# Kernel optimization log

Hardware: AMD Instinct MI355X
Metric: run time of the kernel (lower is better)

Reference implementation:

```python
import jax, jax.numpy as jnp
import numpy as np

G = 256       # number of graphs in batch
NPG = 400     # nodes per graph (hardcoded in module)
DEG = 32      # avg degree
FIN = 400     # input feature dim
H = 64        # hidden_channels
N = G * NPG
E = G * NPG * DEG


def _glorot(key, fan_in, fan_out):
    lim = float(np.sqrt(6.0 / (fan_in + fan_out)))
    return jax.random.uniform(key, (fan_in, fan_out), jnp.float32, -lim, lim)


def setup_inputs() -> dict:
    key = jax.random.key(0)
    ks = jax.random.split(key, 12)
    x = jax.random.normal(ks[0], (N, FIN), jnp.float32)
    # intra-graph random edges, then offset by graph id so edges never cross graphs
    src = jax.random.randint(ks[1], (G, NPG * DEG), 0, NPG)
    dst = jax.random.randint(ks[2], (G, NPG * DEG), 0, NPG)
    offs = (jnp.arange(G) * NPG)[:, None]
    edge_index = jnp.stack([(src + offs).reshape(-1), (dst + offs).reshape(-1)]).astype(jnp.int32)
    edge_weight = jax.random.uniform(ks[3], (E,), jnp.float32)
    return {
        "x": x,
        "edge_index": edge_index,
        "edge_weight": edge_weight,
        "W1": _glorot(ks[4], FIN, H), "b1": jnp.zeros((H,), jnp.float32),
        "W2": _glorot(ks[5], H, H),   "b2": jnp.zeros((H,), jnp.float32),
        "W3": _glorot(ks[6], H, H),   "b3": jnp.zeros((H,), jnp.float32),
        "Wc": _glorot(ks[7], NPG * H, H), "bc": jnp.zeros((H,), jnp.float32),
        "Wl": _glorot(ks[8], H, 2),   "bl": jnp.zeros((2,), jnp.float32),
    }


def _gcn_conv(x, W, b, row, col, norm, n):
    # PyG GCNConv: out[col] += norm * (x @ W)[row]; then + bias
    h = x @ W                                   # [n, out]
    msg = norm[:, None] * h[row]                # [E+n, out] gather + scale
    return jax.ops.segment_sum(msg, col, num_segments=n) + b


def reference(x, edge_index, edge_weight, W1, b1, W2, b2, W3, b3, Wc, bc, Wl, bl):
    n = x.shape[0]
    loop = jnp.arange(n, dtype=edge_index.dtype)
    row = jnp.concatenate([edge_index[0], loop])            # sources (with self-loops)
    col = jnp.concatenate([edge_index[1], loop])            # targets
    ew = jnp.concatenate([edge_weight, jnp.ones((n,), edge_weight.dtype)])
    # symmetric normalization: deg^{-1/2}[row] * w * deg^{-1/2}[col]
    deg = jax.ops.segment_sum(ew, col, num_segments=n)
    dinv = jnp.where(deg > 0, jax.lax.rsqrt(deg), 0.0)
    norm = dinv[row] * ew * dinv[col]

    h = jax.nn.relu(_gcn_conv(x, W1, b1, row, col, norm, n))
    h = jax.nn.relu(_gcn_conv(h, W2, b2, row, col, norm, n))
    h = _gcn_conv(h, W3, b3, row, col, norm, n)
    # per-graph flatten of 400 nodes -> lincomb (vectorized form of the Python loop)
    g = h.reshape(-1, NPG * H) @ Wc + bc        # [G, H]
    # dropout p=0.5 skipped (eval mode)
    return g @ Wl + bl                          # [G, 2]
```

## Files before the change

kernel.cpp:

```cpp
#include <hip/hip_runtime.h>
#include <hip/hip_bf16.h>
#include <stdint.h>

#define G 256
#define NPG 400
#define DEG 32
#define FIN 400
#define H 64
#define NN (G*NPG)
#define EE (G*NPG*DEG)
#define EPG (NPG*DEG)
#define CPG (EPG+NPG)
#define NTILE 25
#define ATS 420
#define HTS 72
#define MTF 26624

#define W1F_OFF 0
#define W1F_N   (13*4*64*8)
#define W2F_OFF (W1F_OFF + W1F_N)
#define W2F_N   (2*4*64*8)
#define W3F_OFF (W2F_OFF + W2F_N)
#define WCF_OFF (W3F_OFF + W2F_N)
#define WCF_N   (832*4*64*8)
#define WF_TOT  (WCF_OFF + WCF_N)

typedef __attribute__((ext_vector_type(8))) _Float16 h8;
typedef __attribute__((ext_vector_type(4))) float f32x4;

static __device__ __forceinline__ unsigned packh2(float a, float b) {
  unsigned short ua = __builtin_bit_cast(unsigned short, (_Float16)a);
  unsigned short ub = __builtin_bit_cast(unsigned short, (_Float16)b);
  return (unsigned)ua | ((unsigned)ub << 16);
}

static __device__ __forceinline__ h8 cvt8(float4 a, float4 b) {
  h8 r;
  r[0] = (_Float16)a.x; r[1] = (_Float16)a.y; r[2] = (_Float16)a.z; r[3] = (_Float16)a.w;
  r[4] = (_Float16)b.x; r[5] = (_Float16)b.y; r[6] = (_Float16)b.z; r[7] = (_Float16)b.w;
  return r;
}

__global__ __launch_bounds__(256) void kPack(
    const float* __restrict__ W1, const float* __restrict__ W2,
    const float* __restrict__ W3, const float* __restrict__ Wc,
    _Float16* __restrict__ wf)
{
  int idx = blockIdx.x*256 + threadIdx.x;
  if (idx >= WF_TOT) return;
  if (idx < W2F_OFF) {
    int i = idx;
    int j = i & 7, ln = (i >> 3) & 63, nt = (i >> 9) & 3, ks = i >> 11;
    int k = ks*32 + (ln >> 4)*8 + j, col = nt*16 + (ln & 15);
    wf[idx] = (k < FIN) ? (_Float16)W1[k*H + col] : (_Float16)0.f;
  } else if (idx < W3F_OFF) {
    int i = idx - W2F_OFF;
    int j = i & 7, ln = (i >> 3) & 63, nt = (i >> 9) & 3, ks = i >> 11;
    wf[idx] = (_Float16)W2[(ks*32 + (ln >> 4)*8 + j)*H + nt*16 + (ln & 15)];
  } else if (idx < WCF_OFF) {
    int i = idx - W3F_OFF;
    int j = i & 7, ln = (i >> 3) & 63, nt = (i >> 9) & 3, ks = i >> 11;
    wf[idx] = (_Float16)W3[(ks*32 + (ln >> 4)*8 + j)*H + nt*16 + (ln & 15)];
  } else {
    int i = idx - WCF_OFF;
    int j = i & 7, ln = (i >> 3) & 63, ntc = (i >> 9) & 3, kt = i >> 11;
    int kp = kt*32 + (ln >> 4)*8 + j;
    int nt_m = kp / 6656, rem = kp % 6656;
    int ks_m = rem >> 9, rem2 = rem & 511;
    int lane_m = rem2 >> 3, j_m = rem2 & 7;
    int node = ks_m*32 + (lane_m >> 4)*8 + j_m;
    int feat = nt_m*16 + (lane_m & 15);
    int col = ntc*16 + (ln & 15);
    wf[idx] = (node < NPG) ? (_Float16)Wc[((size_t)node*64 + feat)*64 + col]
                           : (_Float16)0.f;
  }
}

__global__ __launch_bounds__(1024) void kNorm(
    const int* __restrict__ ei, const float* __restrict__ ew,
    uint32_t* __restrict__ ent, uint32_t* __restrict__ boff)
{
  __shared__ float deg[NPG];
  __shared__ float dv[NPG];
  __shared__ uint32_t bcnt[32], bpos[32];
  const int g = blockIdx.x, tid = threadIdx.x;
  const int ebase = g*EPG, nbase = g*NPG;
  const int* rowp = ei;
  const int* colp = ei + EE;
  if (tid < NTILE) bcnt[tid] = 0u;
  for (int v = tid; v < NPG; v += 1024) deg[v] = 1.0f;
  __syncthreads();
  for (int e = tid; e < EPG; e += 1024) {
    int c = colp[ebase+e] - nbase;
    atomicAdd(&deg[c], ew[ebase+e]);
    atomicAdd(&bcnt[c >> 4], 1u);
  }
  __syncthreads();
  for (int v = tid; v < NPG; v += 1024) dv[v] = rsqrtf(deg[v]);
  if (tid == 0) {
    uint32_t s = 0;
    #pragma unroll
    for (int t = 0; t < NTILE; ++t) {
      uint32_t c = bcnt[t] + 16u;
      bcnt[t] = s; bpos[t] = s; s += c;
    }
  }
  __syncthreads();
  if (tid < NTILE) boff[g*32 + tid] = bcnt[tid];
  if (tid == NTILE) boff[g*32 + NTILE] = (uint32_t)CPG;
  uint32_t* eb = ent + (size_t)g*CPG;
  for (int e = tid; e < EPG; e += 1024) {
    int src = rowp[ebase+e] - nbase;
    int dst = colp[ebase+e] - nbase;
    float nm = dv[src] * ew[ebase+e] * dv[dst];
    unsigned short nb = __builtin_bit_cast(unsigned short, (_Float16)nm);
    uint32_t p = atomicAdd(&bpos[dst >> 4], 1u);
    eb[p] = ((unsigned)(dst & 15) << 26) | ((unsigned)src << 16) | nb;
  }
  for (int v = tid; v < NPG; v += 1024) {
    float nm = dv[v]*dv[v];
    unsigned short nb = __builtin_bit_cast(unsigned short, (_Float16)nm);
    uint32_t p = atomicAdd(&bpos[v >> 4], 1u);
    eb[p] = ((unsigned)(v & 15) << 26) | ((unsigned)v << 16) | nb;
  }
}

__global__ __launch_bounds__(256, 8) void kM1(
    const float* __restrict__ x, const _Float16* __restrict__ wf,
    _Float16* __restrict__ mt1)
{
  const int tid = threadIdx.x, lane = tid & 63, wave = tid >> 6;
  const int l15 = lane & 15, kgrp = lane >> 4;
  const int g = blockIdx.y, b = blockIdx.x;
  const int node_l = b*64 + wave*16 + l15;
  const int arow = (node_l < NPG) ? node_l : NPG-1;
  const float* xp = x + ((size_t)g*NPG + arow)*FIN;

  f32x4 acc[4] = {{0,0,0,0},{0,0,0,0},{0,0,0,0},{0,0,0,0}};
  for (int ks = 0; ks < 13; ++ks) {
    const int kb = ks*32 + kgrp*8;
    h8 af;
    if (kb + 8 <= FIN) {
      float4 a0 = *(const float4*)(xp + kb);
      float4 a1 = *(const float4*)(xp + kb + 4);
      af = cvt8(a0, a1);
    } else {
      h8 z;
      #pragma unroll
      for (int j = 0; j < 8; ++j) z[j] = (_Float16)0.f;
      af = z;
    }
    #pragma unroll
    for (int nt = 0; nt < 4; ++nt) {
      h8 bf = *(const h8*)&wf[W1F_OFF + (((size_t)ks*4 + nt)*64 + lane)*8];
      acc[nt] = __builtin_amdgcn_mfma_f32_16x16x32_f16(af, bf, acc[nt], 0, 0, 0);
    }
  }
  const int nd0 = b*64 + wave*16 + kgrp*4;
  if (nd0 < NPG) {
    const int ksw = nd0 >> 5, lh = (nd0 >> 3) & 3, jb = nd0 & 7;
    _Float16* mb = mt1 + (size_t)g*MTF;
    #pragma unroll
    for (int nt = 0; nt < 4; ++nt) {
      uint2 u;
      u.x = packh2(acc[nt][0], acc[nt][1]);
      u.y = packh2(acc[nt][2], acc[nt][3]);
      *(uint2*)&mb[(((size_t)nt*13 + ksw)*64 + lh*16 + l15)*8 + jb] = u;
    }
  }
}

template<int WMUL>
__global__ __launch_bounds__(256, 4) void kAgg(
    const _Float16* __restrict__ mtin, const _Float16* __restrict__ wfn,
    const float* __restrict__ bias,
    const uint32_t* __restrict__ ent, const uint32_t* __restrict__ boff,
    _Float16* __restrict__ out)
{
  extern __shared__ char smem[];
  float* sAT = (float*)smem;
  _Float16* sh = (_Float16*)(smem + 16*ATS*4);
  const int tid = threadIdx.x, lane = tid & 63;
  const int l15 = lane & 15, kgrp = lane >> 4;
  const int bid = blockIdx.x;
  const int g = bid & 255, t = bid >> 8;
  const int nt = tid >> 6;
  const uint32_t* eb = ent + (size_t)g*CPG;
  const uint32_t s0 = boff[g*32 + t], s1 = boff[g*32 + t + 1];

  h8 BF[13];
  const _Float16* mrow = mtin + (size_t)g*MTF + (size_t)nt*13*512 + lane*8;
  #pragma unroll
  for (int ks = 0; ks < 13; ++ks)
    BF[ks] = *(const h8*)(mrow + ks*512);
  const float bv = bias[nt*16 + l15];
  h8 WF2[2];
  if (WMUL) {
    WF2[0] = *(const h8*)&wfn[((size_t)(0*4 + nt)*64 + lane)*8];
    WF2[1] = *(const h8*)&wfn[((size_t)(1*4 + nt)*64 + lane)*8];
  }
  const uint32_t e0 = s0 + tid;
  uint32_t E0 = 0, E1 = 0, E2 = 0;
  bool p0 = e0 < s1, p1 = e0 + 256 < s1, p2 = e0 + 512 < s1;
  if (p0) E0 = eb[e0];
  if (p1) E1 = eb[e0 + 256];
  if (p2) E2 = eb[e0 + 512];

  { float4* p = (float4*)sAT;
    for (int i = tid; i < 16*ATS/4; i += 256) p[i] = make_float4(0,0,0,0); }
  __syncthreads();

  if (p0) atomicAdd(&sAT[(int)(E0 >> 26)*ATS + (int)((E0 >> 16) & 0x3FFu)],
                    (float)__builtin_bit_cast(_Float16, (unsigned short)(E0 & 0xFFFFu)));
  if (p1) atomicAdd(&sAT[(int)(E1 >> 26)*ATS + (int)((E1 >> 16) & 0x3FFu)],
                    (float)__builtin_bit_cast(_Float16, (unsigned short)(E1 & 0xFFFFu)));
  if (p2) atomicAdd(&sAT[(int)(E2 >> 26)*ATS + (int)((E2 >> 16) & 0x3FFu)],
                    (float)__builtin_bit_cast(_Float16, (unsigned short)(E2 & 0xFFFFu)));
  for (uint32_t e = e0 + 768; e < s1; e += 256) {
    uint32_t E = eb[e];
    atomicAdd(&sAT[(int)(E >> 26)*ATS + (int)((E >> 16) & 0x3FFu)],
              (float)__builtin_bit_cast(_Float16, (unsigned short)(E & 0xFFFFu)));
  }
  __syncthreads();

  f32x4 acc = {0,0,0,0};
  const float* ap = &sAT[l15*ATS];
  #pragma unroll
  for (int ks = 0; ks < 13; ++ks) {
    int kb = ks*32 + kgrp*8;
    float4 a0 = *(const float4*)(ap + kb);
    float4 a1 = *(const float4*)(ap + kb + 4);
    acc = __builtin_amdgcn_mfma_f32_16x16x32_f16(cvt8(a0, a1), BF[ks], acc, 0, 0, 0);
  }

  const int nd0 = t*16 + kgrp*4;
  const int ksw = nd0 >> 5, lh = (nd0 >> 3) & 3, jb = nd0 & 7;
  _Float16* ob = out + (size_t)g*MTF;

  if (!WMUL) {
    uint2 u;
    u.x = packh2(acc[0] + bv, acc[1] + bv);
    u.y = packh2(acc[2] + bv, acc[3] + bv);
    *(uint2*)&ob[(((size_t)nt*13 + ksw)*64 + lh*16 + l15)*8 + jb] = u;
  } else {
    #pragma unroll
    for (int r = 0; r < 4; ++r)
      sh[(kgrp*4 + r)*HTS + nt*16 + l15] = (_Float16)fmaxf(acc[r] + bv, 0.f);
    __syncthreads();
    f32x4 acc2 = {0,0,0,0};
    const _Float16* hp = &sh[l15*HTS];
    acc2 = __builtin_amdgcn_mfma_f32_16x16x32_f16(*(const h8*)(hp + kgrp*8),      WF2[0], acc2, 0, 0, 0);
    acc2 = __builtin_amdgcn_mfma_f32_16x16x32_f16(*(const h8*)(hp + 32 + kgrp*8), WF2[1], acc2, 0, 0, 0);
    uint2 u;
    u.x = packh2(acc2[0], acc2[1]);
    u.y = packh2(acc2[2], acc2[3]);
    *(uint2*)&ob[(((size_t)nt*13 + ksw)*64 + lh*16 + l15)*8 + jb] = u;
  }
}

__global__ __launch_bounds__(256) void kRead(
    const _Float16* __restrict__ h3, const _Float16* __restrict__ wfc,
    float* __restrict__ gpart)
{
  const int tid = threadIdx.x, lane = tid & 63, nt = tid >> 6;
  const int l15 = lane & 15, kgrp = lane >> 4;
  const int rt = blockIdx.x & 15, kc = blockIdx.x >> 4;
  f32x4 acc = {0,0,0,0};
  const _Float16* hp = h3 + (size_t)(rt*16 + l15)*MTF;
  for (int ks = 0; ks < 26; ++ks) {
    int kt = kc*26 + ks;
    h8 af = *(const h8*)(hp + kt*32 + kgrp*8);
    h8 bf = *(const h8*)(wfc + (((size_t)kt*4 + nt)*64 + lane)*8);
    acc = __builtin_amdgcn_mfma_f32_16x16x32_f16(af, bf, acc, 0, 0, 0);
  }
  #pragma unroll
  for (int r = 0; r < 4; ++r)
    gpart[((size_t)(kc*16 + rt)*16 + kgrp*4 + r)*64 + nt*16 + l15] = acc[r];
}

__global__ __launch_bounds__(64) void k6_final(
    const float* __restrict__ gpart, const float* __restrict__ bc,
    const float* __restrict__ Wl, const float* __restrict__ bl,
    float* __restrict__ out)
{
  const int g = blockIdx.x, f = threadIdx.x;
  float s = bc[f];
  #pragma unroll 4
  for (int kc = 0; kc < 32; ++kc)
    s += gpart[((size_t)(kc*16 + (g >> 4))*16 + (g & 15))*64 + f];
  float p0 = s * Wl[f*2 + 0];
  float p1 = s * Wl[f*2 + 1];
  #pragma unroll
  for (int d = 1; d < 64; d <<= 1) {
    p0 += __shfl_xor(p0, d);
    p1 += __shfl_xor(p1, d);
  }
  if (f == 0) {
    out[g*2 + 0] = p0 + bl[0];
    out[g*2 + 1] = p1 + bl[1];
  }
}

extern "C" void kernel_launch(void* const* d_in, const int* in_sizes, int n_in,
                              void* d_out, int out_size, void* d_ws, size_t ws_size,
                              hipStream_t stream)
{
  const float* x  = (const float*)d_in[0];
  const int*   ei = (const int*)d_in[1];
  const float* ew = (const float*)d_in[2];
  const float* W1 = (const float*)d_in[3];
  const float* b1 = (const float*)d_in[4];
  const float* W2 = (const float*)d_in[5];
  const float* b2 = (const float*)d_in[6];
  const float* W3 = (const float*)d_in[7];
  const float* b3 = (const float*)d_in[8];
  const float* Wc = (const float*)d_in[9];
  const float* bc = (const float*)d_in[10];
  const float* Wl = (const float*)d_in[11];
  const float* bl = (const float*)d_in[12];
  float* out = (float*)d_out;
  (void)ws_size;

  char* ws = (char*)d_ws;
  size_t o = 0;
  uint32_t*  ent   = (uint32_t*)(ws + o);  o += (size_t)G*CPG*4;
  uint32_t*  boff  = (uint32_t*)(ws + o);  o += (size_t)G*32*4;
  _Float16*  mtA   = (_Float16*)(ws + o);  o += (size_t)G*MTF*2 + 256;
  _Float16*  mtB   = (_Float16*)(ws + o);  o += (size_t)G*MTF*2 + 256;
  _Float16*  wf    = (_Float16*)(ws + o);  o += (size_t)WF_TOT*2;
  float*     gpart = (float*)(ws + o);     o += (size_t)32*G*H*4;

  kPack<<<(WF_TOT+255)/256, 256, 0, stream>>>(W1, W2, W3, Wc, wf);
  kNorm<<<G, 1024, 0, stream>>>(ei, ew, ent, boff);
  kM1<<<dim3(7, G), 256, 0, stream>>>(x, wf, mtA);
  const int aggLds = 16*ATS*4 + 16*HTS*2;
  kAgg<1><<<NTILE*G, 256, aggLds, stream>>>(mtA, wf + W2F_OFF, b1, ent, boff, mtB);
  kAgg<1><<<NTILE*G, 256, aggLds, stream>>>(mtB, wf + W3F_OFF, b2, ent, boff, mtA);
  kAgg<0><<<NTILE*G, 256, aggLds, stream>>>(mtA, wf, b3, ent, boff, mtB);
  kRead<<<512, 256, 0, stream>>>(mtB, wf + WCF_OFF, gpart);
  k6_final<<<G, 64, 0, stream>>>(gpart, bc, Wl, bl, out);
}
```

Before: 254.7 us.

## Merge pack/norm kernels, fuse final reduction into kRead via atomics, raise kAgg occupancy

Merges the weight-packing kernel and the degree-normalisation kernel into a single launch, with extra blocks doing the packing and zeroing an accumulation buffer. The per-chunk partial sums in kRead are now accumulated with float atomics, and the last block (detected via an atomic counter) computes the final linear layer, which removes the k6_final launch. kAgg launch bounds are raised to request 5 waves per SIMD. The aim is fewer launches and less intermediate traffic, at the cost of atomic contention, nondeterministic summation order and possible register pressure in kAgg.

```diff
diff --git a/kernel.cpp b/kernel.cpp
--- a/kernel.cpp
+++ b/kernel.cpp
@@ -41,49 +41,52 @@
   return r;
 }
 
-__global__ __launch_bounds__(256) void kPack(
+__global__ __launch_bounds__(1024) void kFront(
+    const int* __restrict__ ei, const float* __restrict__ ew,
     const float* __restrict__ W1, const float* __restrict__ W2,
     const float* __restrict__ W3, const float* __restrict__ Wc,
-    _Float16* __restrict__ wf)
-{
-  int idx = blockIdx.x*256 + threadIdx.x;
-  if (idx >= WF_TOT) return;
-  if (idx < W2F_OFF) {
-    int i = idx;
-    int j = i & 7, ln = (i >> 3) & 63, nt = (i >> 9) & 3, ks = i >> 11;
-    int k = ks*32 + (ln >> 4)*8 + j, col = nt*16 + (ln & 15);
-    wf[idx] = (k < FIN) ? (_Float16)W1[k*H + col] : (_Float16)0.f;
-  } else if (idx < W3F_OFF) {
-    int i = idx - W2F_OFF;
-    int j = i & 7, ln = (i >> 3) & 63, nt = (i >> 9) & 3, ks = i >> 11;
-    wf[idx] = (_Float16)W2[(ks*32 + (ln >> 4)*8 + j)*H + nt*16 + (ln & 15)];
-  } else if (idx < WCF_OFF) {
-    int i = idx - W3F_OFF;
-    int j = i & 7, ln = (i >> 3) & 63, nt = (i >> 9) & 3, ks = i >> 11;
-    wf[idx] = (_Float16)W3[(ks*32 + (ln >> 4)*8 + j)*H + nt*16 + (ln & 15)];
-  } else {
-    int i = idx - WCF_OFF;
-    int j = i & 7, ln = (i >> 3) & 63, ntc = (i >> 9) & 3, kt = i >> 11;
-    int kp = kt*32 + (ln >> 4)*8 + j;
-    int nt_m = kp / 6656, rem = kp % 6656;
-    int ks_m = rem >> 9, rem2 = rem & 511;
-    int lane_m = rem2 >> 3, j_m = rem2 & 7;
-    int node = ks_m*32 + (lane_m >> 4)*8 + j_m;
-    int feat = nt_m*16 + (lane_m & 15);
-    int col = ntc*16 + (ln & 15);
-    wf[idx] = (node < NPG) ? (_Float16)Wc[((size_t)node*64 + feat)*64 + col]
-                           : (_Float16)0.f;
-  }
-}
-
-__global__ __launch_bounds__(1024) void kNorm(
-    const int* __restrict__ ei, const float* __restrict__ ew,
-    uint32_t* __restrict__ ent, uint32_t* __restrict__ boff)
+    uint32_t* __restrict__ ent, uint32_t* __restrict__ boff,
+    _Float16* __restrict__ wf, float* __restrict__ gbuf, uint32_t* __restrict__ cnt)
 {
   __shared__ float deg[NPG];
   __shared__ float dv[NPG];
   __shared__ uint32_t bcnt[32], bpos[32];
-  const int g = blockIdx.x, tid = threadIdx.x;
+  const int b = blockIdx.x, tid = threadIdx.x;
+
+  if (b >= 256) {
+    int idx = (b - 256)*1024 + tid;
+    if (idx < G*H) gbuf[idx] = 0.f;
+    if (idx == 0) *cnt = 0u;
+    if (idx < W2F_OFF) {
+      int i = idx;
+      int j = i & 7, ln = (i >> 3) & 63, nt = (i >> 9) & 3, ks = i >> 11;
+      int k = ks*32 + (ln >> 4)*8 + j, col = nt*16 + (ln & 15);
+      wf[idx] = (k < FIN) ? (_Float16)W1[k*H + col] : (_Float16)0.f;
+    } else if (idx < W3F_OFF) {
+      int i = idx - W2F_OFF;
+      int j = i & 7, ln = (i >> 3) & 63, nt = (i >> 9) & 3, ks = i >> 11;
+      wf[idx] = (_Float16)W2[(ks*32 + (ln >> 4)*8 + j)*H + nt*16 + (ln & 15)];
+    } else if (idx < WCF_OFF) {
+      int i = idx - W3F_OFF;
+      int j = i & 7, ln = (i >> 3) & 63, nt = (i >> 9) & 3, ks = i >> 11;
+      wf[idx] = (_Float16)W3[(ks*32 + (ln >> 4)*8 + j)*H + nt*16 + (ln & 15)];
+    } else {
+      int i = idx - WCF_OFF;
+      int j = i & 7, ln = (i >> 3) & 63, ntc = (i >> 9) & 3, kt = i >> 11;
+      int kp = kt*32 + (ln >> 4)*8 + j;
+      int nt_m = kp / 6656, rem = kp % 6656;
+      int ks_m = rem >> 9, rem2 = rem & 511;
+      int lane_m = rem2 >> 3, j_m = rem2 & 7;
+      int node = ks_m*32 + (lane_m >> 4)*8 + j_m;
+      int feat = nt_m*16 + (lane_m & 15);
+      int col = ntc*16 + (ln & 15);
+      wf[idx] = (node < NPG) ? (_Float16)Wc[((size_t)node*64 + feat)*64 + col]
+                             : (_Float16)0.f;
+    }
+    return;
+  }
+
+  const int g = b;
   const int ebase = g*EPG, nbase = g*NPG;
   const int* rowp = ei;
   const int* colp = ei + EE;
@@ -171,7 +174,7 @@
 }
 
 template<int WMUL>
-__global__ __launch_bounds__(256, 4) void kAgg(
+__global__ __launch_bounds__(256, 5) void kAgg(
     const _Float16* __restrict__ mtin, const _Float16* __restrict__ wfn,
     const float* __restrict__ bias,
     const uint32_t* __restrict__ ent, const uint32_t* __restrict__ boff,
@@ -260,8 +263,11 @@
 
 __global__ __launch_bounds__(256) void kRead(
     const _Float16* __restrict__ h3, const _Float16* __restrict__ wfc,
-    float* __restrict__ gpart)
-{
+    float* __restrict__ gbuf, uint32_t* __restrict__ cnt,
+    const float* __restrict__ bc, const float* __restrict__ Wl,
+    const float* __restrict__ bl, float* __restrict__ out)
+{
+  __shared__ uint32_t sdone;
   const int tid = threadIdx.x, lane = tid & 63, nt = tid >> 6;
   const int l15 = lane & 15, kgrp = lane >> 4;
   const int rt = blockIdx.x & 15, kc = blockIdx.x >> 4;
@@ -275,29 +281,29 @@
   }
   #pragma unroll
   for (int r = 0; r < 4; ++r)
-    gpart[((size_t)(kc*16 + rt)*16 + kgrp*4 + r)*64 + nt*16 + l15] = acc[r];
-}
-
-__global__ __launch_bounds__(64) void k6_final(
-    const float* __restrict__ gpart, const float* __restrict__ bc,
-    const float* __restrict__ Wl, const float* __restrict__ bl,
-    float* __restrict__ out)
-{
-  const int g = blockIdx.x, f = threadIdx.x;
-  float s = bc[f];
-  #pragma unroll 4
-  for (int kc = 0; kc < 32; ++kc)
-    s += gpart[((size_t)(kc*16 + (g >> 4))*16 + (g & 15))*64 + f];
-  float p0 = s * Wl[f*2 + 0];
-  float p1 = s * Wl[f*2 + 1];
-  #pragma unroll
-  for (int d = 1; d < 64; d <<= 1) {
-    p0 += __shfl_xor(p0, d);
-    p1 += __shfl_xor(p1, d);
-  }
-  if (f == 0) {
-    out[g*2 + 0] = p0 + bl[0];
-    out[g*2 + 1] = p1 + bl[1];
+    atomicAdd(&gbuf[(size_t)(rt*16 + kgrp*4 + r)*H + nt*16 + l15], acc[r]);
+  __threadfence();
+  if (tid == 0)
+    sdone = __hip_atomic_fetch_add(cnt, 1u, __ATOMIC_ACQ_REL, __HIP_MEMORY_SCOPE_AGENT);
+  __syncthreads();
+  if (sdone != 511u) return;
+
+  const float wl0 = Wl[lane*2 + 0], wl1 = Wl[lane*2 + 1];
+  const float bcv = bc[lane];
+  for (int gg = nt*64; gg < nt*64 + 64; ++gg) {
+    float v = __hip_atomic_load(&gbuf[(size_t)gg*H + lane],
+                                __ATOMIC_RELAXED, __HIP_MEMORY_SCOPE_AGENT);
+    float s = v + bcv;
+    float p0 = s * wl0, p1 = s * wl1;
+    #pragma unroll
+    for (int d = 1; d < 64; d <<= 1) {
+      p0 += __shfl_xor(p0, d);
+      p1 += __shfl_xor(p1, d);
+    }
+    if (lane == 0) {
+      out[gg*2 + 0] = p0 + bl[0];
+      out[gg*2 + 1] = p1 + bl[1];
+    }
   }
 }
 
@@ -328,15 +334,15 @@
   _Float16*  mtA   = (_Float16*)(ws + o);  o += (size_t)G*MTF*2 + 256;
   _Float16*  mtB   = (_Float16*)(ws + o);  o += (size_t)G*MTF*2 + 256;
   _Float16*  wf    = (_Float16*)(ws + o);  o += (size_t)WF_TOT*2;
-  float*     gpart = (float*)(ws + o);     o += (size_t)32*G*H*4;
-
-  kPack<<<(WF_TOT+255)/256, 256, 0, stream>>>(W1, W2, W3, Wc, wf);
-  kNorm<<<G, 1024, 0, stream>>>(ei, ew, ent, boff);
+  float*     gbuf  = (float*)(ws + o);     o += (size_t)G*H*4;
+  uint32_t*  cnt   = (uint32_t*)(ws + o);  o += 256;
+
+  kFront<<<256 + WF_TOT/1024, 1024, 0, stream>>>(ei, ew, W1, W2, W3, Wc,
+                                                 ent, boff, wf, gbuf, cnt);
   kM1<<<dim3(7, G), 256, 0, stream>>>(x, wf, mtA);
   const int aggLds = 16*ATS*4 + 16*HTS*2;
   kAgg<1><<<NTILE*G, 256, aggLds, stream>>>(mtA, wf + W2F_OFF, b1, ent, boff, mtB);
   kAgg<1><<<NTILE*G, 256, aggLds, stream>>>(mtB, wf + W3F_OFF, b2, ent, boff, mtA);
   kAgg<0><<<NTILE*G, 256, aggLds, stream>>>(mtA, wf, b3, ent, boff, mtB);
-  kRead<<<512, 256, 0, stream>>>(mtB, wf + WCF_OFF, gpart);
-  k6_final<<<G, 64, 0, stream>>>(gpart, bc, Wl, bl, out);
-}
+  kRead<<<512, 256, 0, stream>>>(mtB, wf + WCF_OFF, gbuf, cnt, bc, Wl, bl, out);
+}
```

Result: slower. 320.6 us (+25.9%).
